# Kernel tuning notes

Measured on AMD Instinct MI355X. Metric: run time of the kernel, lower is better.

## Reference

```python
import jax, jax.numpy as jnp
import numpy as np

N_NODES = 100000
N_EDGES = 3200000
N_GRAPHS = 3200

def setup_inputs() -> dict:
    key = jax.random.key(0)
    ks = jax.random.split(key, 12)
    def glorot(k, shape):
        lim = np.sqrt(6.0 / (shape[0] + shape[1]))
        return jax.random.uniform(k, shape, jnp.float32, -lim, lim)
    x = jax.random.normal(ks[0], (N_NODES, 37), jnp.float32)
    edge_index = jax.random.randint(ks[1], (2, N_EDGES), 0, N_NODES, jnp.int64 if jax.config.jax_enable_x64 else jnp.int32)
    batch = jnp.sort(jax.random.randint(ks[2], (N_NODES,), 0, N_GRAPHS))
    return {
        'x': x,
        'W1': glorot(ks[3], (37, 128)),  'b1': jnp.zeros((128,), jnp.float32),
        'W2': glorot(ks[4], (128, 256)), 'b2': jnp.zeros((256,), jnp.float32),
        'W3': glorot(ks[5], (256, 256)), 'b3': jnp.zeros((256,), jnp.float32),
        'Wp': glorot(ks[6], (256, 256)), 'bp': jnp.zeros((256,), jnp.float32),
        'edge_index': edge_index,
        'batch': batch,
    }

def _gcn_conv(h, W, b, src, dst, dis):
    # PyG GCNConv: h' = D^{-1/2}(A+I)D^{-1/2} (h W) + b, self-loops added
    hW = h @ W
    norm = dis[src] * dis[dst]                      # [E]
    msg = hW[src] * norm[:, None]                   # gather + scale
    agg = jax.ops.segment_sum(msg, dst, num_segments=N_NODES)
    agg = agg + hW * (dis * dis)[:, None]           # self-loop contribution
    return agg + b

def reference(x, W1, b1, W2, b2, W3, b3, Wp, bp, edge_index, batch):
    src, dst = edge_index[0], edge_index[1]
    # degree with self-loops (all edge weights = 1)
    deg = jax.ops.segment_sum(jnp.ones((N_EDGES,), x.dtype), dst, num_segments=N_NODES) + 1.0
    dis = jax.lax.rsqrt(deg)
    h = jax.nn.relu(_gcn_conv(x, W1, b1, src, dst, dis))
    h = jax.nn.relu(_gcn_conv(h, W2, b2, src, dst, dis))
    h = jax.nn.relu(_gcn_conv(h, W3, b3, src, dst, dis))
    # global mean pool over graphs
    sums = jax.ops.segment_sum(h, batch, num_segments=N_GRAPHS)
    cnts = jax.ops.segment_sum(jnp.ones((N_NODES,), x.dtype), batch, num_segments=N_GRAPHS)
    pooled = sums / jnp.maximum(cnts, 1.0)[:, None]
    return pooled @ Wp + bp
```

## Files before the change

kernel.cpp:

```cpp
#include <hip/hip_runtime.h>

#define N_NODES  100000
#define N_EDGES  3200000
#define N_GRAPHS 3200

#define NBLK 200
#define EB   16000
#define BSH  7
#define NB   ((N_NODES + 127) >> BSH)
#define BCAP 5120

typedef __attribute__((ext_vector_type(8))) short bf16x8;
typedef __attribute__((ext_vector_type(4))) float f32x4;

__device__ __forceinline__ float bf2f(unsigned short u) {
    return __uint_as_float(((unsigned)u) << 16);
}
__device__ __forceinline__ unsigned short f2bf(float f) {
    unsigned u = __float_as_uint(f);
    u += 0x7fffu + ((u >> 16) & 1u);
    return (unsigned short)(u >> 16);
}


__global__ __launch_bounds__(256, 4)
void hist_kernel(const int* __restrict__ dst, int* __restrict__ hist) {
    __shared__ int lh[NB];
    int blk = blockIdx.x, t = threadIdx.x;
    for (int b = t; b < NB; b += 256) lh[b] = 0;
    __syncthreads();
    int e0 = blk * EB;
    for (int i = t; i < EB; i += 256)
        atomicAdd(&lh[dst[e0 + i] >> BSH], 1);
    __syncthreads();
    for (int b = t; b < NB; b += 256) hist[b * NBLK + blk] = lh[b];
}

__global__ void bucket_tot_kernel(const int* __restrict__ hist, int* __restrict__ tot) {
    int b = blockIdx.x, l = threadIdx.x;
    int s = 0;
    for (int k = l; k < NBLK; k += 64) s += hist[b * NBLK + k];
    for (int off = 32; off; off >>= 1) s += __shfl_down(s, off);
    if (l == 0) tot[b] = s;
}

__global__ void bucket_scan_kernel(const int* __restrict__ tot, int* __restrict__ bucketStart) {
    __shared__ int part[256];
    int t = threadIdx.x;
    int chunk = (NB + 255) / 256;
    int lo = t * chunk; if (lo > NB) lo = NB;
    int hi = lo + chunk; if (hi > NB) hi = NB;
    int s = 0;
    for (int i = lo; i < hi; ++i) s += tot[i];
    part[t] = s;
    __syncthreads();
    for (int off = 1; off < 256; off <<= 1) {
        int v = part[t];
        int a = (t >= off) ? part[t - off] : 0;
        __syncthreads();
        part[t] = v + a;
        __syncthreads();
    }
    int run = (t == 0) ? 0 : part[t - 1];
    for (int i = lo; i < hi; ++i) { bucketStart[i] = run; run += tot[i]; }
    if (t == 255) bucketStart[NB] = run;
}

__global__ void bucket_base_kernel(int* __restrict__ hist, const int* __restrict__ bucketStart) {
    int b = blockIdx.x * blockDim.x + threadIdx.x;
    if (b >= NB) return;
    int run = bucketStart[b];
    int* row = hist + b * NBLK;
#pragma unroll 4
    for (int k = 0; k < NBLK; ++k) { int v = row[k]; row[k] = run; run += v; }
}

__global__ __launch_bounds__(256, 4)
void scatter1_kernel(const int* __restrict__ src, const int* __restrict__ dst,
                     const int* __restrict__ base,
                     int* __restrict__ sdst, int* __restrict__ ssrc) {
    __shared__ int lcur[NB];
    int blk = blockIdx.x, t = threadIdx.x;
    for (int b = t; b < NB; b += 256) lcur[b] = base[b * NBLK + blk];
    __syncthreads();
    int e0 = blk * EB;
    for (int i = t; i < EB; i += 256) {
        int d = dst[e0 + i], s = src[e0 + i];
        int pos = atomicAdd(&lcur[d >> BSH], 1);
        sdst[pos] = d;
        ssrc[pos] = s;
    }
}

__global__ __launch_bounds__(256, 1)
void csr2_kernel(const int* __restrict__ sdst, const int* __restrict__ ssrc,
                 const int* __restrict__ bucketStart,
                 int* __restrict__ offsets, float* __restrict__ dis,
                 int* __restrict__ csr_src) {
    __shared__ int ldst[BCAP];
    __shared__ int lsrc[BCAP];
    __shared__ int lhist[128], loff[128], lcur[128];
    int b = blockIdx.x, t = threadIdx.x;
    int n0 = b << BSH;
    int e0 = bucketStart[b], e1 = bucketStart[b + 1];
    int cnt = e1 - e0; if (cnt > BCAP) cnt = BCAP;
    for (int i = t; i < cnt; i += 256) {
        ldst[i] = sdst[e0 + i] - n0;
        lsrc[i] = ssrc[e0 + i];
    }
    if (t < 128) lhist[t] = 0;
    __syncthreads();
    for (int i = t; i < cnt; i += 256) atomicAdd(&lhist[ldst[i]], 1);
    __syncthreads();
    if (t < 128) loff[t] = lhist[t];
    __syncthreads();
    for (int off = 1; off < 128; off <<= 1) {
        int v = 0;
        if (t < 128) { v = loff[t]; if (t >= off) v += loff[t - off]; }
        __syncthreads();
        if (t < 128) loff[t] = v;
        __syncthreads();
    }
    if (t < 128) {
        int excl = loff[t] - lhist[t];
        lcur[t] = excl;
        int n = n0 + t;
        if (n < N_NODES) {
            offsets[n] = e0 + excl;
            dis[n] = rsqrtf((float)lhist[t] + 1.0f);
        }
    }
    if (b == 0 && t == 0) offsets[N_NODES] = N_EDGES;
    __syncthreads();
    for (int i = t; i < cnt; i += 256) {
        int pos = atomicAdd(&lcur[ldst[i]], 1);
        csr_src[e0 + pos] = lsrc[i];
    }
}

template<int K>
__global__ void pack_w_kernel(const float* __restrict__ W,
                              unsigned short* __restrict__ hi,
                              unsigned short* __restrict__ lo) {
    constexpr int KS = K / 32;
    int idx = blockIdx.x * blockDim.x + threadIdx.x;
    if (idx >= 16 * KS * 64) return;
    int l = idx & 63;
    int s = (idx >> 6) % KS;
    int t = idx / (64 * KS);
    int k0 = s * 32 + (l >> 4) * 8;
    int n  = t * 16 + (l & 15);
    size_t base = (size_t)idx * 8;
#pragma unroll
    for (int j = 0; j < 8; ++j) {
        float w = W[(size_t)(k0 + j) * 256 + n];
        unsigned short h = f2bf(w);
        float rem = w - bf2f(h);
        hi[base + j] = h;
        lo[base + j] = f2bf(rem);
    }
}

__global__ __launch_bounds__(128, 2)
void gemm1_kernel(const float* __restrict__ x, const float* __restrict__ W,
                  const float* __restrict__ dis, unsigned short* __restrict__ out) {
    __shared__ float lds[16 * 37];
    int row0 = blockIdx.x * 16;
    int t = threadIdx.x;
    const float* src = x + (size_t)row0 * 37;
    for (int i = t; i < 16 * 37; i += 128) lds[i] = src[i];
    __syncthreads();
    float acc[16];
#pragma unroll
    for (int r = 0; r < 16; ++r) acc[r] = 0.0f;
#pragma unroll
    for (int k = 0; k < 37; ++k) {
        float wv = W[k * 128 + t];
#pragma unroll
        for (int r = 0; r < 16; ++r) acc[r] += lds[r * 37 + k] * wv;
    }
#pragma unroll
    for (int r = 0; r < 16; ++r) {
        int row = row0 + r;
        out[(size_t)row * 128 + t] = f2bf(acc[r] * dis[row]);
    }
}

template<int F, bool FINISH>
__global__ __launch_bounds__(256, 4)
void agg_bf16_kernel(const unsigned short* __restrict__ tab,
                     const int* __restrict__ csr_src,
                     const int* __restrict__ offsets,
                     const float* __restrict__ dis,
                     const float* __restrict__ bias,
                     unsigned short* __restrict__ out) {
    int wave = threadIdx.x >> 6;
    int lane = threadIdx.x & 63;
    int n = blockIdx.x * 4 + wave;

    float acc[F / 64];
    if (F == 128) {
        ushort2 u = ((const ushort2*)(tab + (size_t)n * F))[lane];
        acc[0] = bf2f(u.x); acc[1] = bf2f(u.y);
    } else {
        ushort4 u = ((const ushort4*)(tab + (size_t)n * F))[lane];
        acc[0] = bf2f(u.x); acc[1] = bf2f(u.y); acc[2] = bf2f(u.z); acc[3] = bf2f(u.w);
    }

    int lo = offsets[n], hi = offsets[n + 1];
    int j = lo;
    for (; j + 16 <= hi; j += 16) {
        int sidx[16];
#pragma unroll
        for (int u = 0; u < 16; ++u) sidx[u] = csr_src[j + u];
        if (F == 128) {
            ushort2 v[16];
#pragma unroll
            for (int u = 0; u < 16; ++u)
                v[u] = ((const ushort2*)(tab + (size_t)sidx[u] * F))[lane];
#pragma unroll
            for (int u = 0; u < 16; ++u) { acc[0] += bf2f(v[u].x); acc[1] += bf2f(v[u].y); }
        } else {
            ushort4 v[16];
#pragma unroll
            for (int u = 0; u < 16; ++u)
                v[u] = ((const ushort4*)(tab + (size_t)sidx[u] * F))[lane];
#pragma unroll
            for (int u = 0; u < 16; ++u) {
                acc[0] += bf2f(v[u].x); acc[1] += bf2f(v[u].y);
                acc[2] += bf2f(v[u].z); acc[3] += bf2f(v[u].w);
            }
        }
    }
    for (; j + 4 <= hi; j += 4) {
        int sidx[4];
#pragma unroll
        for (int u = 0; u < 4; ++u) sidx[u] = csr_src[j + u];
        if (F == 128) {
            ushort2 v[4];
#pragma unroll
            for (int u = 0; u < 4; ++u)
                v[u] = ((const ushort2*)(tab + (size_t)sidx[u] * F))[lane];
#pragma unroll
            for (int u = 0; u < 4; ++u) { acc[0] += bf2f(v[u].x); acc[1] += bf2f(v[u].y); }
        } else {
            ushort4 v[4];
#pragma unroll
            for (int u = 0; u < 4; ++u)
                v[u] = ((const ushort4*)(tab + (size_t)sidx[u] * F))[lane];
#pragma unroll
            for (int u = 0; u < 4; ++u) {
                acc[0] += bf2f(v[u].x); acc[1] += bf2f(v[u].y);
                acc[2] += bf2f(v[u].z); acc[3] += bf2f(v[u].w);
            }
        }
    }
    for (; j < hi; ++j) {
        int s = csr_src[j];
        if (F == 128) {
            ushort2 u = ((const ushort2*)(tab + (size_t)s * F))[lane];
            acc[0] += bf2f(u.x); acc[1] += bf2f(u.y);
        } else {
            ushort4 u = ((const ushort4*)(tab + (size_t)s * F))[lane];
            acc[0] += bf2f(u.x); acc[1] += bf2f(u.y); acc[2] += bf2f(u.z); acc[3] += bf2f(u.w);
        }
    }

    float d = dis[n];
    if (F == 128) {
        ushort2 o;
        if (FINISH) {
            o.x = f2bf(fmaxf(d * acc[0] + bias[lane * 2 + 0], 0.0f) * d);
            o.y = f2bf(fmaxf(d * acc[1] + bias[lane * 2 + 1], 0.0f) * d);
        } else {
            o.x = f2bf(d * acc[0]); o.y = f2bf(d * acc[1]);
        }
        ((ushort2*)(out + (size_t)n * F))[lane] = o;
    } else {
        ushort4 o;
        if (FINISH) {
            o.x = f2bf(fmaxf(d * acc[0] + bias[lane * 4 + 0], 0.0f) * d);
            o.y = f2bf(fmaxf(d * acc[1] + bias[lane * 4 + 1], 0.0f) * d);
            o.z = f2bf(fmaxf(d * acc[2] + bias[lane * 4 + 2], 0.0f) * d);
            o.w = f2bf(fmaxf(d * acc[3] + bias[lane * 4 + 3], 0.0f) * d);
        } else {
            o.x = f2bf(d * acc[0]); o.y = f2bf(d * acc[1]);
            o.z = f2bf(d * acc[2]); o.w = f2bf(d * acc[3]);
        }
        ((ushort4*)(out + (size_t)n * F))[lane] = o;
    }
}

template<int K, int MODE>
__global__ __launch_bounds__(256, 4)
void mfma_gemm_kernel(const unsigned short* __restrict__ A,
                      const unsigned short* __restrict__ Bhi,
                      const unsigned short* __restrict__ Blo,
                      const float* __restrict__ bias,
                      const float* __restrict__ dis,
                      void* __restrict__ outv) {
    constexpr int KS = K / 32;
    int l   = threadIdx.x & 63;
    int wid = threadIdx.x >> 6;
    int n0  = wid * 64;
    int m0  = blockIdx.x * 32;

    f32x4 acc0[4], acc1[4];
#pragma unroll
    for (int tn = 0; tn < 4; ++tn) { acc0[tn] = (f32x4){0,0,0,0}; acc1[tn] = (f32x4){0,0,0,0}; }

    const unsigned short* a0 = A + (size_t)(m0 + (l & 15)) * K + (l >> 4) * 8;
    const unsigned short* a1 = a0 + (size_t)16 * K;

#pragma unroll
    for (int s = 0; s < KS; ++s) {
        bf16x8 af0 = *(const bf16x8*)(a0 + s * 32);
        bf16x8 af1 = *(const bf16x8*)(a1 + s * 32);
#pragma unroll
        for (int tn = 0; tn < 4; ++tn) {
            int t = (n0 >> 4) + tn;
            size_t boff = ((size_t)(t * KS + s) * 64 + l) * 8;
            bf16x8 bh = *(const bf16x8*)(Bhi + boff);
            bf16x8 bl = *(const bf16x8*)(Blo + boff);
            acc0[tn] = __builtin_amdgcn_mfma_f32_16x16x32_bf16(af0, bh, acc0[tn], 0, 0, 0);
            acc0[tn] = __builtin_amdgcn_mfma_f32_16x16x32_bf16(af0, bl, acc0[tn], 0, 0, 0);
            acc1[tn] = __builtin_amdgcn_mfma_f32_16x16x32_bf16(af1, bh, acc1[tn], 0, 0, 0);
            acc1[tn] = __builtin_amdgcn_mfma_f32_16x16x32_bf16(af1, bl, acc1[tn], 0, 0, 0);
        }
    }

    int rowg = (l >> 4) * 4;
#pragma unroll
    for (int tn = 0; tn < 4; ++tn) {
        int n = n0 + tn * 16 + (l & 15);
        float b = bias[n];
#pragma unroll
        for (int r = 0; r < 4; ++r) {
#pragma unroll
            for (int half = 0; half < 2; ++half) {
                int m = m0 + half * 16 + rowg + r;
                float v = fmaxf((half ? acc1[tn][r] : acc0[tn][r]) + b, 0.0f);
                if (MODE == 1)      ((unsigned short*)outv)[(size_t)m * 256 + n] = f2bf(v * dis[m]);
                else if (MODE == 2) ((unsigned short*)outv)[(size_t)m * 256 + n] = f2bf(v);
                else                ((float*)outv)[(size_t)m * 256 + n] = v;
            }
        }
    }
}

__device__ __forceinline__ int lower_bound_dev(const int* __restrict__ a, int n, int key) {
    int lo = 0, hi = n;
    while (lo < hi) {
        int mid = (lo + hi) >> 1;
        if (a[mid] < key) lo = mid + 1; else hi = mid;
    }
    return lo;
}

__global__ __launch_bounds__(256, 4)
void pool_bf16_kernel(const unsigned short* __restrict__ h, const int* __restrict__ batch,
                      float* __restrict__ pooled) {
    int wave = threadIdx.x >> 6;
    int lane = threadIdx.x & 63;
    int g = blockIdx.x * 4 + wave;
    int lo = lower_bound_dev(batch, N_NODES, g);
    int hi = lower_bound_dev(batch, N_NODES, g + 1);
    float a0 = 0, a1 = 0, a2 = 0, a3 = 0;
    for (int n = lo; n < hi; ++n) {
        ushort4 u = ((const ushort4*)(h + (size_t)n * 256))[lane];
        a0 += bf2f(u.x); a1 += bf2f(u.y); a2 += bf2f(u.z); a3 += bf2f(u.w);
    }
    float inv = 1.0f / fmaxf((float)(hi - lo), 1.0f);
    float4 o = {a0 * inv, a1 * inv, a2 * inv, a3 * inv};
    *(float4*)&pooled[(size_t)g * 256 + lane * 4] = o;
}

__global__ __launch_bounds__(256, 2)
void head_gemm_kernel(const float* __restrict__ H, const float* __restrict__ W,
                      const float* __restrict__ bias, float* __restrict__ out) {
    __shared__ float lds[16 * 256];
    int row0 = blockIdx.x * 16;
    int t = threadIdx.x;
    const float* src = H + (size_t)row0 * 256;
    for (int i = t; i < 16 * 256; i += 256) lds[i] = src[i];
    __syncthreads();
    float acc[16];
#pragma unroll
    for (int r = 0; r < 16; ++r) acc[r] = 0.0f;
#pragma unroll 4
    for (int k = 0; k < 256; ++k) {
        float wv = W[k * 256 + t];
#pragma unroll
        for (int r = 0; r < 16; ++r) acc[r] += lds[r * 256 + k] * wv;
    }
#pragma unroll
    for (int r = 0; r < 16; ++r)
        out[(size_t)(row0 + r) * 256 + t] = acc[r] + bias[t];
}

static inline size_t align_up(size_t x, size_t a) { return (x + a - 1) & ~(a - 1); }

extern "C" void kernel_launch(void* const* d_in, const int* in_sizes, int n_in,
                              void* d_out, int out_size, void* d_ws, size_t ws_size,
                              hipStream_t stream) {
    const float* x  = (const float*)d_in[0];
    const float* W1 = (const float*)d_in[1];
    const float* b1 = (const float*)d_in[2];
    const float* W2 = (const float*)d_in[3];
    const float* b2 = (const float*)d_in[4];
    const float* W3 = (const float*)d_in[5];
    const float* b3 = (const float*)d_in[6];
    const float* Wp = (const float*)d_in[7];
    const float* bp = (const float*)d_in[8];
    const int*   ei = (const int*)d_in[9];
    const int*   batch = (const int*)d_in[10];
    float* out = (float*)d_out;

    const int* e_src = ei;
    const int* e_dst = ei + N_EDGES;

    char* p = (char*)d_ws;
    size_t off = 0;
    auto take = [&](size_t bytes) {
        void* r = p + off;
        off = align_up(off + bytes, 256);
        return r;
    };
    int*   hist        = (int*)  take(sizeof(int) * NB * NBLK);
    int*   tot         = (int*)  take(sizeof(int) * NB);
    int*   bucketStart = (int*)  take(sizeof(int) * (NB + 1));
    int*   offsets     = (int*)  take(sizeof(int) * (N_NODES + 1));
    int*   csr_src     = (int*)  take(sizeof(int) * N_EDGES);
    float* dis         = (float*)take(sizeof(float) * N_NODES);
    float* pooled      = (float*)take(sizeof(float) * N_GRAPHS * 256);
    unsigned short* whi2 = (unsigned short*)take(sizeof(unsigned short) * 128 * 256);
    unsigned short* wlo2 = (unsigned short*)take(sizeof(unsigned short) * 128 * 256);
    unsigned short* whi3 = (unsigned short*)take(sizeof(unsigned short) * 256 * 256);
    unsigned short* wlo3 = (unsigned short*)take(sizeof(unsigned short) * 256 * 256);
    unsigned short* bufX = (unsigned short*)take(sizeof(unsigned short) * (size_t)N_NODES * 256);
    unsigned short* bufY = (unsigned short*)take(sizeof(unsigned short) * (size_t)N_NODES * 256);
    unsigned short* h3   = (unsigned short*)take(sizeof(unsigned short) * (size_t)N_NODES * 256);

    int* sdst = (int*)h3;
    int* ssrc = sdst + N_EDGES;

    unsigned short* t1     = bufX;
    unsigned short* table2 = bufX + (size_t)N_NODES * 128;
    unsigned short* pbuf2  = bufX;
    unsigned short* table3 = bufY;
    unsigned short* pbuf3  = bufX;

    hist_kernel<<<NBLK, 256, 0, stream>>>(e_dst, hist);
    bucket_tot_kernel<<<NB, 64, 0, stream>>>(hist, tot);
    bucket_scan_kernel<<<1, 256, 0, stream>>>(tot, bucketStart);
    bucket_base_kernel<<<(NB + 255) / 256, 256, 0, stream>>>(hist, bucketStart);
    scatter1_kernel<<<NBLK, 256, 0, stream>>>(e_src, e_dst, hist, sdst, ssrc);
    csr2_kernel<<<NB, 256, 0, stream>>>(sdst, ssrc, bucketStart, offsets, dis, csr_src);

    pack_w_kernel<128><<<(16 * 4 * 64 + 255) / 256, 256, 0, stream>>>(W2, whi2, wlo2);
    pack_w_kernel<256><<<(16 * 8 * 64 + 255) / 256, 256, 0, stream>>>(W3, whi3, wlo3);

    gemm1_kernel<<<N_NODES / 16, 128, 0, stream>>>(x, W1, dis, t1);
    agg_bf16_kernel<128, true><<<N_NODES / 4, 256, 0, stream>>>(t1, csr_src, offsets, dis, b1, table2);

    agg_bf16_kernel<128, false><<<N_NODES / 4, 256, 0, stream>>>(table2, csr_src, offsets, dis, nullptr, pbuf2);
    mfma_gemm_kernel<128, 1><<<N_NODES / 32, 256, 0, stream>>>(pbuf2, whi2, wlo2, b2, dis, table3);

    agg_bf16_kernel<256, false><<<N_NODES / 4, 256, 0, stream>>>(table3, csr_src, offsets, dis, nullptr, pbuf3);
    mfma_gemm_kernel<256, 2><<<N_NODES / 32, 256, 0, stream>>>(pbuf3, whi3, wlo3, b3, nullptr, h3);

    pool_bf16_kernel<<<N_GRAPHS / 4, 256, 0, stream>>>(h3, batch, pooled);
    head_gemm_kernel<<<N_GRAPHS / 16, 256, 0, stream>>>(pooled, Wp, bp, out);
}
```

Before: 737.8 us.

## Reorder layer 1 to aggregate first, sort edges by source tile, stagger start

Layer 1 now casts x (padded to 64 columns, pre-scaled by dis) to bf16, aggregates at width 64 and then runs an MFMA GEMM, instead of transforming to 128 first and aggregating at width 128. The CSR build also sorts each node's neighbours by source-node tile (4096-node bins) and stores 26 offsets per node. Aggregation starts each node's neighbour walk at a point staggered by block index, so concurrent waves touch different source regions and gathers should get better cache locality. The costs are a larger per-node offset table, extra shared memory and atomics in csr2, and one extra kernel launch for layer 1.

```diff
diff --git a/kernel.cpp b/kernel.cpp
--- a/kernel.cpp
+++ b/kernel.cpp
@@ -9,6 +9,9 @@
 #define BSH  7
 #define NB   ((N_NODES + 127) >> BSH)
 #define BCAP 5120
+#define NT   25
+#define TSH  12
+#define TP   33
 
 typedef __attribute__((ext_vector_type(8))) short bf16x8;
 typedef __attribute__((ext_vector_type(4))) float f32x4;
@@ -95,24 +98,34 @@
 __global__ __launch_bounds__(256, 1)
 void csr2_kernel(const int* __restrict__ sdst, const int* __restrict__ ssrc,
                  const int* __restrict__ bucketStart,
-                 int* __restrict__ offsets, float* __restrict__ dis,
+                 int* __restrict__ tileoff, float* __restrict__ dis,
                  int* __restrict__ csr_src) {
-    __shared__ int ldst[BCAP];
+    __shared__ int lkey[BCAP];
     __shared__ int lsrc[BCAP];
-    __shared__ int lhist[128], loff[128], lcur[128];
+    __shared__ int lh[128 * TP];
+    __shared__ int lc[128 * TP];
+    __shared__ int loff[128], ldeg[128];
     int b = blockIdx.x, t = threadIdx.x;
     int n0 = b << BSH;
     int e0 = bucketStart[b], e1 = bucketStart[b + 1];
     int cnt = e1 - e0; if (cnt > BCAP) cnt = BCAP;
     for (int i = t; i < cnt; i += 256) {
-        ldst[i] = sdst[e0 + i] - n0;
-        lsrc[i] = ssrc[e0 + i];
-    }
-    if (t < 128) lhist[t] = 0;
-    __syncthreads();
-    for (int i = t; i < cnt; i += 256) atomicAdd(&lhist[ldst[i]], 1);
-    __syncthreads();
-    if (t < 128) loff[t] = lhist[t];
+        int d = sdst[e0 + i] - n0;
+        int s = ssrc[e0 + i];
+        lkey[i] = d * TP + (s >> TSH);
+        lsrc[i] = s;
+    }
+    for (int i = t; i < 128 * TP; i += 256) lh[i] = 0;
+    __syncthreads();
+    for (int i = t; i < cnt; i += 256) atomicAdd(&lh[lkey[i]], 1);
+    __syncthreads();
+    if (t < 128) {
+        int run = 0;
+#pragma unroll
+        for (int p = 0; p < NT; ++p) { lc[t * TP + p] = run; run += lh[t * TP + p]; }
+        ldeg[t] = run;
+        loff[t] = run;
+    }
     __syncthreads();
     for (int off = 1; off < 128; off <<= 1) {
         int v = 0;
@@ -122,29 +135,36 @@
         __syncthreads();
     }
     if (t < 128) {
-        int excl = loff[t] - lhist[t];
-        lcur[t] = excl;
+        int excl = loff[t] - ldeg[t];
         int n = n0 + t;
         if (n < N_NODES) {
-            offsets[n] = e0 + excl;
-            dis[n] = rsqrtf((float)lhist[t] + 1.0f);
-        }
-    }
-    if (b == 0 && t == 0) offsets[N_NODES] = N_EDGES;
+#pragma unroll
+            for (int p = 0; p < NT; ++p) {
+                int v = lc[t * TP + p] + excl;
+                lc[t * TP + p] = v;
+                tileoff[(size_t)n * 26 + p] = e0 + v;
+            }
+            tileoff[(size_t)n * 26 + NT] = e0 + excl + ldeg[t];
+            dis[n] = rsqrtf((float)ldeg[t] + 1.0f);
+        } else {
+#pragma unroll
+            for (int p = 0; p < NT; ++p) lc[t * TP + p] += excl;
+        }
+    }
     __syncthreads();
     for (int i = t; i < cnt; i += 256) {
-        int pos = atomicAdd(&lcur[ldst[i]], 1);
+        int pos = atomicAdd(&lc[lkey[i]], 1);
         csr_src[e0 + pos] = lsrc[i];
     }
 }
 
-template<int K>
-__global__ void pack_w_kernel(const float* __restrict__ W,
+template<int K, int N>
+__global__ void pack_w_kernel(const float* __restrict__ W, int Krows,
                               unsigned short* __restrict__ hi,
                               unsigned short* __restrict__ lo) {
     constexpr int KS = K / 32;
     int idx = blockIdx.x * blockDim.x + threadIdx.x;
-    if (idx >= 16 * KS * 64) return;
+    if (idx >= (N / 16) * KS * 64) return;
     int l = idx & 63;
     int s = (idx >> 6) % KS;
     int t = idx / (64 * KS);
@@ -153,7 +173,8 @@
     size_t base = (size_t)idx * 8;
 #pragma unroll
     for (int j = 0; j < 8; ++j) {
-        float w = W[(size_t)(k0 + j) * 256 + n];
+        int k = k0 + j;
+        float w = (k < Krows) ? W[(size_t)k * N + n] : 0.0f;
         unsigned short h = f2bf(w);
         float rem = w - bf2f(h);
         hi[base + j] = h;
@@ -161,45 +182,106 @@
     }
 }
 
-__global__ __launch_bounds__(128, 2)
-void gemm1_kernel(const float* __restrict__ x, const float* __restrict__ W,
-                  const float* __restrict__ dis, unsigned short* __restrict__ out) {
-    __shared__ float lds[16 * 37];
-    int row0 = blockIdx.x * 16;
-    int t = threadIdx.x;
-    const float* src = x + (size_t)row0 * 37;
-    for (int i = t; i < 16 * 37; i += 128) lds[i] = src[i];
-    __syncthreads();
-    float acc[16];
-#pragma unroll
-    for (int r = 0; r < 16; ++r) acc[r] = 0.0f;
-#pragma unroll
-    for (int k = 0; k < 37; ++k) {
-        float wv = W[k * 128 + t];
-#pragma unroll
-        for (int r = 0; r < 16; ++r) acc[r] += lds[r * 37 + k] * wv;
-    }
-#pragma unroll
-    for (int r = 0; r < 16; ++r) {
-        int row = row0 + r;
-        out[(size_t)row * 128 + t] = f2bf(acc[r] * dis[row]);
-    }
-}
-
-template<int F, bool FINISH>
+__global__ __launch_bounds__(256, 4)
+void cast_x_kernel(const float* __restrict__ x, const float* __restrict__ dis,
+                   unsigned short* __restrict__ xb) {
+    int idx = blockIdx.x * blockDim.x + threadIdx.x;
+    if (idx >= N_NODES * 64) return;
+    int n = idx >> 6, c = idx & 63;
+    xb[idx] = (c < 37) ? f2bf(x[(size_t)n * 37 + c] * dis[n]) : (unsigned short)0;
+}
+
+template<int F>
+__device__ __forceinline__ void agg_range(const unsigned short* __restrict__ tab,
+                                          const int* __restrict__ csr_src,
+                                          int j, int hi, int lane, float* acc) {
+    for (; j + 16 <= hi; j += 16) {
+        int sidx[16];
+#pragma unroll
+        for (int u = 0; u < 16; ++u) sidx[u] = csr_src[j + u];
+        if (F == 64) {
+            unsigned short v[16];
+#pragma unroll
+            for (int u = 0; u < 16; ++u) v[u] = tab[(size_t)sidx[u] * 64 + lane];
+#pragma unroll
+            for (int u = 0; u < 16; ++u) acc[0] += bf2f(v[u]);
+        } else if (F == 128) {
+            ushort2 v[16];
+#pragma unroll
+            for (int u = 0; u < 16; ++u)
+                v[u] = ((const ushort2*)(tab + (size_t)sidx[u] * F))[lane];
+#pragma unroll
+            for (int u = 0; u < 16; ++u) { acc[0] += bf2f(v[u].x); acc[1] += bf2f(v[u].y); }
+        } else {
+            ushort4 v[16];
+#pragma unroll
+            for (int u = 0; u < 16; ++u)
+                v[u] = ((const ushort4*)(tab + (size_t)sidx[u] * F))[lane];
+#pragma unroll
+            for (int u = 0; u < 16; ++u) {
+                acc[0] += bf2f(v[u].x); acc[1] += bf2f(v[u].y);
+                acc[2] += bf2f(v[u].z); acc[3] += bf2f(v[u].w);
+            }
+        }
+    }
+    for (; j + 4 <= hi; j += 4) {
+        int sidx[4];
+#pragma unroll
+        for (int u = 0; u < 4; ++u) sidx[u] = csr_src[j + u];
+        if (F == 64) {
+            unsigned short v[4];
+#pragma unroll
+            for (int u = 0; u < 4; ++u) v[u] = tab[(size_t)sidx[u] * 64 + lane];
+#pragma unroll
+            for (int u = 0; u < 4; ++u) acc[0] += bf2f(v[u]);
+        } else if (F == 128) {
+            ushort2 v[4];
+#pragma unroll
+            for (int u = 0; u < 4; ++u)
+                v[u] = ((const ushort2*)(tab + (size_t)sidx[u] * F))[lane];
+#pragma unroll
+            for (int u = 0; u < 4; ++u) { acc[0] += bf2f(v[u].x); acc[1] += bf2f(v[u].y); }
+        } else {
+            ushort4 v[4];
+#pragma unroll
+            for (int u = 0; u < 4; ++u)
+                v[u] = ((const ushort4*)(tab + (size_t)sidx[u] * F))[lane];
+#pragma unroll
+            for (int u = 0; u < 4; ++u) {
+                acc[0] += bf2f(v[u].x); acc[1] += bf2f(v[u].y);
+                acc[2] += bf2f(v[u].z); acc[3] += bf2f(v[u].w);
+            }
+        }
+    }
+    for (; j < hi; ++j) {
+        int s = csr_src[j];
+        if (F == 64) {
+            acc[0] += bf2f(tab[(size_t)s * 64 + lane]);
+        } else if (F == 128) {
+            ushort2 u = ((const ushort2*)(tab + (size_t)s * F))[lane];
+            acc[0] += bf2f(u.x); acc[1] += bf2f(u.y);
+        } else {
+            ushort4 u = ((const ushort4*)(tab + (size_t)s * F))[lane];
+            acc[0] += bf2f(u.x); acc[1] += bf2f(u.y); acc[2] += bf2f(u.z); acc[3] += bf2f(u.w);
+        }
+    }
+}
+
+template<int F>
 __global__ __launch_bounds__(256, 4)
 void agg_bf16_kernel(const unsigned short* __restrict__ tab,
                      const int* __restrict__ csr_src,
-                     const int* __restrict__ offsets,
+                     const int* __restrict__ tileoff,
                      const float* __restrict__ dis,
-                     const float* __restrict__ bias,
                      unsigned short* __restrict__ out) {
     int wave = threadIdx.x >> 6;
     int lane = threadIdx.x & 63;
     int n = blockIdx.x * 4 + wave;
 
-    float acc[F / 64];
-    if (F == 128) {
+    float acc[(F + 63) / 64];
+    if (F == 64) {
+        acc[0] = bf2f(tab[(size_t)n * 64 + lane]);
+    } else if (F == 128) {
         ushort2 u = ((const ushort2*)(tab + (size_t)n * F))[lane];
         acc[0] = bf2f(u.x); acc[1] = bf2f(u.y);
     } else {
@@ -207,107 +289,45 @@
         acc[0] = bf2f(u.x); acc[1] = bf2f(u.y); acc[2] = bf2f(u.z); acc[3] = bf2f(u.w);
     }
 
-    int lo = offsets[n], hi = offsets[n + 1];
-    int j = lo;
-    for (; j + 16 <= hi; j += 16) {
-        int sidx[16];
-#pragma unroll
-        for (int u = 0; u < 16; ++u) sidx[u] = csr_src[j + u];
-        if (F == 128) {
-            ushort2 v[16];
-#pragma unroll
-            for (int u = 0; u < 16; ++u)
-                v[u] = ((const ushort2*)(tab + (size_t)sidx[u] * F))[lane];
-#pragma unroll
-            for (int u = 0; u < 16; ++u) { acc[0] += bf2f(v[u].x); acc[1] += bf2f(v[u].y); }
-        } else {
-            ushort4 v[16];
-#pragma unroll
-            for (int u = 0; u < 16; ++u)
-                v[u] = ((const ushort4*)(tab + (size_t)sidx[u] * F))[lane];
-#pragma unroll
-            for (int u = 0; u < 16; ++u) {
-                acc[0] += bf2f(v[u].x); acc[1] += bf2f(v[u].y);
-                acc[2] += bf2f(v[u].z); acc[3] += bf2f(v[u].w);
-            }
-        }
-    }
-    for (; j + 4 <= hi; j += 4) {
-        int sidx[4];
-#pragma unroll
-        for (int u = 0; u < 4; ++u) sidx[u] = csr_src[j + u];
-        if (F == 128) {
-            ushort2 v[4];
-#pragma unroll
-            for (int u = 0; u < 4; ++u)
-                v[u] = ((const ushort2*)(tab + (size_t)sidx[u] * F))[lane];
-#pragma unroll
-            for (int u = 0; u < 4; ++u) { acc[0] += bf2f(v[u].x); acc[1] += bf2f(v[u].y); }
-        } else {
-            ushort4 v[4];
-#pragma unroll
-            for (int u = 0; u < 4; ++u)
-                v[u] = ((const ushort4*)(tab + (size_t)sidx[u] * F))[lane];
-#pragma unroll
-            for (int u = 0; u < 4; ++u) {
-                acc[0] += bf2f(v[u].x); acc[1] += bf2f(v[u].y);
-                acc[2] += bf2f(v[u].z); acc[3] += bf2f(v[u].w);
-            }
-        }
-    }
-    for (; j < hi; ++j) {
-        int s = csr_src[j];
-        if (F == 128) {
-            ushort2 u = ((const ushort2*)(tab + (size_t)s * F))[lane];
-            acc[0] += bf2f(u.x); acc[1] += bf2f(u.y);
-        } else {
-            ushort4 u = ((const ushort4*)(tab + (size_t)s * F))[lane];
-            acc[0] += bf2f(u.x); acc[1] += bf2f(u.y); acc[2] += bf2f(u.z); acc[3] += bf2f(u.w);
-        }
-    }
+    int lo = tileoff[(size_t)n * 26 + 0];
+    int hi = tileoff[(size_t)n * 26 + NT];
+    int deg = hi - lo;
+    int jsplit = lo + (int)(((long long)deg * blockIdx.x) / gridDim.x);
+
+    agg_range<F>(tab, csr_src, jsplit, hi, lane, acc);
+    agg_range<F>(tab, csr_src, lo, jsplit, lane, acc);
 
     float d = dis[n];
-    if (F == 128) {
-        ushort2 o;
-        if (FINISH) {
-            o.x = f2bf(fmaxf(d * acc[0] + bias[lane * 2 + 0], 0.0f) * d);
-            o.y = f2bf(fmaxf(d * acc[1] + bias[lane * 2 + 1], 0.0f) * d);
-        } else {
-            o.x = f2bf(d * acc[0]); o.y = f2bf(d * acc[1]);
-        }
+    if (F == 64) {
+        out[(size_t)n * 64 + lane] = f2bf(d * acc[0]);
+    } else if (F == 128) {
+        ushort2 o; o.x = f2bf(d * acc[0]); o.y = f2bf(d * acc[1]);
         ((ushort2*)(out + (size_t)n * F))[lane] = o;
     } else {
         ushort4 o;
-        if (FINISH) {
-            o.x = f2bf(fmaxf(d * acc[0] + bias[lane * 4 + 0], 0.0f) * d);
-            o.y = f2bf(fmaxf(d * acc[1] + bias[lane * 4 + 1], 0.0f) * d);
-            o.z = f2bf(fmaxf(d * acc[2] + bias[lane * 4 + 2], 0.0f) * d);
-            o.w = f2bf(fmaxf(d * acc[3] + bias[lane * 4 + 3], 0.0f) * d);
-        } else {
-            o.x = f2bf(d * acc[0]); o.y = f2bf(d * acc[1]);
-            o.z = f2bf(d * acc[2]); o.w = f2bf(d * acc[3]);
-        }
+        o.x = f2bf(d * acc[0]); o.y = f2bf(d * acc[1]);
+        o.z = f2bf(d * acc[2]); o.w = f2bf(d * acc[3]);
         ((ushort4*)(out + (size_t)n * F))[lane] = o;
     }
 }
 
-template<int K, int MODE>
+template<int K, int NTW, int N, int MODE>
 __global__ __launch_bounds__(256, 4)
 void mfma_gemm_kernel(const unsigned short* __restrict__ A,
                       const unsigned short* __restrict__ Bhi,
                       const unsigned short* __restrict__ Blo,
                       const float* __restrict__ bias,
                       const float* __restrict__ dis,
-                      void* __restrict__ outv) {
+                      unsigned short* __restrict__ outv) {
     constexpr int KS = K / 32;
     int l   = threadIdx.x & 63;
     int wid = threadIdx.x >> 6;
-    int n0  = wid * 64;
+    int n0  = wid * (NTW * 16);
     int m0  = blockIdx.x * 32;
 
-    f32x4 acc0[4], acc1[4];
-#pragma unroll
-    for (int tn = 0; tn < 4; ++tn) { acc0[tn] = (f32x4){0,0,0,0}; acc1[tn] = (f32x4){0,0,0,0}; }
+    f32x4 acc0[NTW], acc1[NTW];
+#pragma unroll
+    for (int tn = 0; tn < NTW; ++tn) { acc0[tn] = (f32x4){0,0,0,0}; acc1[tn] = (f32x4){0,0,0,0}; }
 
     const unsigned short* a0 = A + (size_t)(m0 + (l & 15)) * K + (l >> 4) * 8;
     const unsigned short* a1 = a0 + (size_t)16 * K;
@@ -317,7 +337,7 @@
         bf16x8 af0 = *(const bf16x8*)(a0 + s * 32);
         bf16x8 af1 = *(const bf16x8*)(a1 + s * 32);
 #pragma unroll
-        for (int tn = 0; tn < 4; ++tn) {
+        for (int tn = 0; tn < NTW; ++tn) {
             int t = (n0 >> 4) + tn;
             size_t boff = ((size_t)(t * KS + s) * 64 + l) * 8;
             bf16x8 bh = *(const bf16x8*)(Bhi + boff);
@@ -331,7 +351,7 @@
 
     int rowg = (l >> 4) * 4;
 #pragma unroll
-    for (int tn = 0; tn < 4; ++tn) {
+    for (int tn = 0; tn < NTW; ++tn) {
         int n = n0 + tn * 16 + (l & 15);
         float b = bias[n];
 #pragma unroll
@@ -340,9 +360,8 @@
             for (int half = 0; half < 2; ++half) {
                 int m = m0 + half * 16 + rowg + r;
                 float v = fmaxf((half ? acc1[tn][r] : acc0[tn][r]) + b, 0.0f);
-                if (MODE == 1)      ((unsigned short*)outv)[(size_t)m * 256 + n] = f2bf(v * dis[m]);
-                else if (MODE == 2) ((unsigned short*)outv)[(size_t)m * 256 + n] = f2bf(v);
-                else                ((float*)outv)[(size_t)m * 256 + n] = v;
+                if (MODE == 1) outv[(size_t)m * N + n] = f2bf(v * dis[m]);
+                else           outv[(size_t)m * N + n] = f2bf(v);
             }
         }
     }
@@ -429,10 +448,12 @@
     int*   hist        = (int*)  take(sizeof(int) * NB * NBLK);
     int*   tot         = (int*)  take(sizeof(int) * NB);
     int*   bucketStart = (int*)  take(sizeof(int) * (NB + 1));
-    int*   offsets     = (int*)  take(sizeof(int) * (N_NODES + 1));
+    int*   tileoff     = (int*)  take(sizeof(int) * (size_t)N_NODES * 26);
     int*   csr_src     = (int*)  take(sizeof(int) * N_EDGES);
     float* dis         = (float*)take(sizeof(float) * N_NODES);
     float* pooled      = (float*)take(sizeof(float) * N_GRAPHS * 256);
+    unsigned short* whi1 = (unsigned short*)take(sizeof(unsigned short) * 64 * 128);
+    unsigned short* wlo1 = (unsigned short*)take(sizeof(unsigned short) * 64 * 128);
     unsigned short* whi2 = (unsigned short*)take(sizeof(unsigned short) * 128 * 256);
     unsigned short* wlo2 = (unsigned short*)take(sizeof(unsigned short) * 128 * 256);
     unsigned short* whi3 = (unsigned short*)take(sizeof(unsigned short) * 256 * 256);
@@ -444,9 +465,10 @@
     int* sdst = (int*)h3;
     int* ssrc = sdst + N_EDGES;
 
-    unsigned short* t1     = bufX;
-    unsigned short* table2 = bufX + (size_t)N_NODES * 128;
-    unsigned short* pbuf2  = bufX;
+    unsigned short* xb     = bufY;
+    unsigned short* pbuf1  = bufY + (size_t)N_NODES * 64;
+    unsigned short* table2 = bufX;
+    unsigned short* pbuf2  = bufX + (size_t)N_NODES * 128;
     unsigned short* table3 = bufY;
     unsigned short* pbuf3  = bufX;
 
@@ -455,19 +477,21 @@
     bucket_scan_kernel<<<1, 256, 0, stream>>>(tot, bucketStart);
     bucket_base_kernel<<<(NB + 255) / 256, 256, 0, stream>>>(hist, bucketStart);
     scatter1_kernel<<<NBLK, 256, 0, stream>>>(e_src, e_dst, hist, sdst, ssrc);
-    csr2_kernel<<<NB, 256, 0, stream>>>(sdst, ssrc, bucketStart, offsets, dis, csr_src);
-
-    pack_w_kernel<128><<<(16 * 4 * 64 + 255) / 256, 256, 0, stream>>>(W2, whi2, wlo2);
-    pack_w_kernel<256><<<(16 * 8 * 64 + 255) / 256, 256, 0, stream>>>(W3, whi3, wlo3);
-
-    gemm1_kernel<<<N_NODES / 16, 128, 0, stream>>>(x, W1, dis, t1);
-    agg_bf16_kernel<128, true><<<N_NODES / 4, 256, 0, stream>>>(t1, csr_src, offsets, dis, b1, table2);
-
-    agg_bf16_kernel<128, false><<<N_NODES / 4, 256, 0, stream>>>(table2, csr_src, offsets, dis, nullptr, pbuf2);
-    mfma_gemm_kernel<128, 1><<<N_NODES / 32, 256, 0, stream>>>(pbuf2, whi2, wlo2, b2, dis, table3);
-
-    agg_bf16_kernel<256, false><<<N_NODES / 4, 256, 0, stream>>>(table3, csr_src, offsets, dis, nullptr, pbuf3);
-    mfma_gemm_kernel<256, 2><<<N_NODES / 32, 256, 0, stream>>>(pbuf3, whi3, wlo3, b3, nullptr, h3);
+    csr2_kernel<<<NB, 256, 0, stream>>>(sdst, ssrc, bucketStart, tileoff, dis, csr_src);
+
+    pack_w_kernel<64, 128><<<((128 / 16) * 2 * 64 + 255) / 256, 256, 0, stream>>>(W1, 37, whi1, wlo1);
+    pack_w_kernel<128, 256><<<((256 / 16) * 4 * 64 + 255) / 256, 256, 0, stream>>>(W2, 128, whi2, wlo2);
+    pack_w_kernel<256, 256><<<((256 / 16) * 8 * 64 + 255) / 256, 256, 0, stream>>>(W3, 256, whi3, wlo3);
+
+    cast_x_kernel<<<(N_NODES * 64 + 255) / 256, 256, 0, stream>>>(x, dis, xb);
+    agg_bf16_kernel<64><<<N_NODES / 4, 256, 0, stream>>>(xb, csr_src, tileoff, dis, pbuf1);
+    mfma_gemm_kernel<64, 2, 128, 1><<<N_NODES / 32, 256, 0, stream>>>(pbuf1, whi1, wlo1, b1, dis, table2);
+
+    agg_bf16_kernel<128><<<N_NODES / 4, 256, 0, stream>>>(table2, csr_src, tileoff, dis, pbuf2);
+    mfma_gemm_kernel<128, 4, 256, 1><<<N_NODES / 32, 256, 0, stream>>>(pbuf2, whi2, wlo2, b2, dis, table3);
+
+    agg_bf16_kernel<256><<<N_NODES / 4, 256, 0, stream>>>(table3, csr_src, tileoff, dis, pbuf3);
+    mfma_gemm_kernel<256, 4, 256, 2><<<N_NODES / 32, 256, 0, stream>>>(pbuf3, whi3, wlo3, b3, nullptr, h3);
 
     pool_bf16_kernel<<<N_GRAPHS / 4, 256, 0, stream>>>(h3, batch, pooled);
     head_gemm_kernel<<<N_GRAPHS / 16, 256, 0, stream>>>(pooled, Wp, bp, out);
```

New measurement: 739.9 us. Within noise of the previous version (+0.3%).
